# Kernel tuning notes

Hardware: AMD Instinct MI355X
Metric: run time of the kernel (lower is better)

The kernel has to match this reference:

```python
import jax, jax.numpy as jnp
import numpy as np

NBODY = 63          # body 0 = world, body 1 = free-joint root, bodies 2..62 = hinge
NHINGE = NBODY - 2  # 61 hinge dofs -> qpos dim = 7 + 61 = 68
NSITES = 16
B = 131072


def _qmul(q1, q2):
    """Hamilton product, (w,x,y,z) convention. Broadcasts over leading dims."""
    w1, x1, y1, z1 = q1[..., 0], q1[..., 1], q1[..., 2], q1[..., 3]
    w2, x2, y2, z2 = q2[..., 0], q2[..., 1], q2[..., 2], q2[..., 3]
    return jnp.stack([
        w1 * w2 - x1 * x2 - y1 * y2 - z1 * z2,
        w1 * x2 + x1 * w2 + y1 * z2 - z1 * y2,
        w1 * y2 - x1 * z2 + y1 * w2 + z1 * x2,
        w1 * z2 + x1 * y2 - y1 * x2 + z1 * w2,
    ], axis=-1)


def _qrot(q, v):
    """Rotate v by unit quaternion q (equivalent to q*v*q^-1 sandwich)."""
    u = q[..., 1:]
    w = q[..., :1]
    t = 2.0 * jnp.cross(u, v)
    return v + w * t + jnp.cross(u, t)


def setup_inputs() -> dict:
    key = jax.random.key(0)
    ks = jax.random.split(key, 8)
    qpos = jax.random.normal(ks[0], (B, 7 + NHINGE), dtype=jnp.float32) * 0.3
    body_pos = jax.random.normal(ks[1], (NBODY, 3), dtype=jnp.float32) * 0.1
    bq = jax.random.normal(ks[2], (NBODY, 4), dtype=jnp.float32)
    body_quat = bq / jnp.linalg.norm(bq, axis=-1, keepdims=True)
    ax = jax.random.normal(ks[3], (NHINGE, 3), dtype=jnp.float32)
    hinge_axis = ax / jnp.linalg.norm(ax, axis=-1, keepdims=True)
    jnt_pos = jax.random.normal(ks[4], (NHINGE, 3), dtype=jnp.float32) * 0.05
    site_pos = jax.random.normal(ks[5], (NSITES, 3), dtype=jnp.float32) * 0.05
    body_parent = jnp.maximum(jnp.arange(NBODY, dtype=jnp.int32) - 1, 0)  # chain tree
    site_body = jax.random.randint(ks[6], (NSITES,), 1, NBODY, dtype=jnp.int32)
    return {
        'qpos': qpos, 'body_pos': body_pos, 'body_quat': body_quat,
        'hinge_axis': hinge_axis, 'jnt_pos': jnt_pos, 'site_pos': site_pos,
        'body_parent': body_parent, 'site_body': site_body,
    }


def reference(qpos, body_pos, body_quat, hinge_axis, jnt_pos, site_pos,
              body_parent, site_body):
    # Structural ints are static tree topology: pull to host for Python indexing.
    parents = np.asarray(body_parent)
    sbody = np.asarray(site_body)
    Bn = qpos.shape[0]
    nbody = body_pos.shape[0]

    wp = [None] * nbody  # per-body world position [B,3]
    wq = [None] * nbody  # per-body world quaternion [B,4]
    wp[0] = jnp.zeros((Bn, 3), dtype=qpos.dtype)
    wq[0] = jnp.broadcast_to(jnp.array([1.0, 0.0, 0.0, 0.0], dtype=qpos.dtype), (Bn, 4))

    # body 1: free joint -> root pos + normalized quat straight from qpos
    wp[1] = qpos[:, 0:3]
    q = qpos[:, 3:7]
    wq[1] = q / jnp.linalg.norm(q, axis=-1, keepdims=True)

    # hinge bodies, parents always processed before children
    for bid in range(2, nbody):
        h = bid - 2
        p = int(parents[bid])
        half = 0.5 * qpos[:, 7 + h]
        s, c = jnp.sin(half), jnp.cos(half)
        ax = hinge_axis[h]
        hq = jnp.stack([c, s * ax[0], s * ax[1], s * ax[2]], axis=-1)  # [B,4]
        local_combined = _qmul(jnp.broadcast_to(body_quat[bid], (Bn, 4)), hq)
        anchor = wp[p] + _qrot(wq[p], body_pos[bid] + jnt_pos[h])  # world joint anchor
        nq = _qmul(wq[p], local_combined)
        wq[bid] = nq
        wp[bid] = anchor - _qrot(nq, jnt_pos[h])

    WP = jnp.stack(wp, axis=1)  # [B, nbody, 3]
    WQ = jnp.stack(wq, axis=1)  # [B, nbody, 4]

    # sites: vectorized gather + rotate over all keypoint sites at once
    sq = WQ[:, sbody]                         # [B, S, 4]
    sp = WP[:, sbody]                         # [B, S, 3]
    sites = sp + _qrot(sq, site_pos[None, :, :])  # [B, S, 3]
    return sites
```

## Files before the change

kernel.cpp:

```cpp
#include <hip/hip_runtime.h>


#define NBODY  63
#define NHINGE 61
#define NSITES 16
#define QDIM   68
#define LSTRIDE 49
#define INV2PI 0.15915494309189535f

typedef unsigned int u32;

#define HC_OFF   0
#define SP_OFF   (NHINGE * 16)
#define MASK_OFF (SP_OFF + NSITES * 4)
#define BM_OFF   (MASK_OFF + 64)

__global__ void fk_setup(const float* __restrict__ body_pos, const float* __restrict__ body_quat,
                         const float* __restrict__ hinge_axis, const float* __restrict__ jnt_pos,
                         const float* __restrict__ site_pos, const int* __restrict__ site_body,
                         float* __restrict__ ws)
{
    int tid = threadIdx.x;
    if (tid < NHINGE) {
        int h = tid, bid = h + 2;
        float uw = body_quat[bid*4+0], ux = body_quat[bid*4+1];
        float uy = body_quat[bid*4+2], uz = body_quat[bid*4+3];
        float ax = hinge_axis[h*3+0], ay = hinge_axis[h*3+1], az = hinge_axis[h*3+2];
        float jx = jnt_pos[h*3+0],   jy = jnt_pos[h*3+1],   jz = jnt_pos[h*3+2];
        float bx = body_pos[bid*3+0], by = body_pos[bid*3+1], bz = body_pos[bid*3+2];
        float* o = ws + HC_OFF + h * 16;
        o[0] = uw; o[1] = ux; o[2] = uy; o[3] = uz;
        o[4] = -(ux * ax + uy * ay + uz * az);
        o[5] =  uw * ax + uy * az - uz * ay;
        o[6] =  uw * ay - ux * az + uz * ax;
        o[7] =  uw * az + ux * ay - uy * ax;
        o[8] = bx + jx; o[9] = by + jy; o[10] = bz + jz; o[11] = 0.f;
        o[12] = jx; o[13] = jy; o[14] = jz; o[15] = 0.f;
    }
    if (tid < NSITES) {
        float* o = ws + SP_OFF + tid * 4;
        o[0] = site_pos[tid*3+0];
        o[1] = site_pos[tid*3+1];
        o[2] = site_pos[tid*3+2];
        o[3] = 0.f;
    }
    if (tid == 0) {
        int* im = (int*)(ws + MASK_OFF);
        unsigned long long bm = 0ull;
        for (int b = 0; b < NBODY; b++) {
            int m = 0;
            for (int s = 0; s < NSITES; s++)
                if (site_body[s] == b) m |= (1 << s);
            im[b] = m;
            if (m) bm |= (1ull << b);
        }
        u32* pbm = (u32*)(ws + BM_OFF);
        pbm[0] = (u32)bm; pbm[1] = (u32)(bm >> 32);
    }
}

__global__ __launch_bounds__(256, 3)
void fk_main(const float* __restrict__ qpos, const float* __restrict__ ws,
             float* __restrict__ out)
{
    __shared__ float sbuf[256 * LSTRIDE];
    const int tid = threadIdx.x;
    const int t = blockIdx.x * 256 + tid;
    float* my = sbuf + tid * LSTRIDE;
    const float* rowp = qpos + (size_t)t * QDIM;

    const u32* pbm = (const u32*)(ws + BM_OFF);
    unsigned long long bodymask = ((unsigned long long)pbm[1] << 32) | (unsigned long long)pbm[0];
    const int* im = (const int*)(ws + MASK_OFF);

    float4 r0 = *reinterpret_cast<const float4*>(rowp);
    float2 r1 = *reinterpret_cast<const float2*>(rowp + 4);
    float  r2 = rowp[6];
    float wpx = r0.x, wpy = r0.y, wpz = r0.z;
    float qw = r0.w, qx = r1.x, qy = r1.y, qz = r2;
    float inv = rsqrtf(qw * qw + qx * qx + qy * qy + qz * qz);
    qw *= inv; qx *= inv; qy *= inv; qz *= inv;

    auto emit = [&](int bid) {
        int m = im[bid];
        while (m) {
            int s = __ffs(m) - 1; m &= m - 1;
            const float* sp = ws + SP_OFF + s * 4;
            float vx = sp[0], vy = sp[1], vz = sp[2];
            float tx = 2.f * (qy * vz - qz * vy);
            float ty = 2.f * (qz * vx - qx * vz);
            float tz = 2.f * (qx * vy - qy * vx);
            float* o = my + s * 3;
            o[0] = wpx + vx + qw * tx + (qy * tz - qz * ty);
            o[1] = wpy + vy + qw * ty + (qz * tx - qx * tz);
            o[2] = wpz + vz + qw * tz + (qx * ty - qy * tx);
        }
    };

    if (bodymask & 2ull) emit(1);

    float ang = rowp[7];
#pragma unroll 1
    for (int h = 0; h < NHINGE; h++) {
        int nidx = 7 + ((h + 1 < NHINGE) ? (h + 1) : h);
        float angn = rowp[nidx];

        const float* c = ws + HC_OFF + h * 16;
        float rev = (0.5f * INV2PI) * ang;
        float sn = __builtin_amdgcn_sinf(rev);
        float cs = __builtin_amdgcn_cosf(rev);
        float lw = cs * c[0] + sn * c[4];
        float lx = cs * c[1] + sn * c[5];
        float ly = cs * c[2] + sn * c[6];
        float lz = cs * c[3] + sn * c[7];
        float ax = c[8], ay = c[9], az = c[10];
        float tx = 2.f * (qy * az - qz * ay);
        float ty = 2.f * (qz * ax - qx * az);
        float tz = 2.f * (qx * ay - qy * ax);
        float anx = wpx + ax + qw * tx + (qy * tz - qz * ty);
        float any_ = wpy + ay + qw * ty + (qz * tx - qx * tz);
        float anz = wpz + az + qw * tz + (qx * ty - qy * tx);
        float nw = qw * lw - qx * lx - qy * ly - qz * lz;
        float nx = qw * lx + qx * lw + qy * lz - qz * ly;
        float ny = qw * ly - qx * lz + qy * lw + qz * lx;
        float nz = qw * lz + qx * ly - qy * lx + qz * lw;
        float jx = c[12], jy = c[13], jz = c[14];
        float t2x = 2.f * (ny * jz - nz * jy);
        float t2y = 2.f * (nz * jx - nx * jz);
        float t2z = 2.f * (nx * jy - ny * jx);
        wpx = anx - (jx + nw * t2x + (ny * t2z - nz * t2y));
        wpy = any_ - (jy + nw * t2y + (nz * t2x - nx * t2z));
        wpz = anz - (jz + nw * t2z + (nx * t2y - ny * t2x));
        qw = nw; qx = nx; qy = ny; qz = nz;

        if ((bodymask >> (h + 2)) & 1ull) emit(h + 2);
        ang = angn;
    }

    __syncthreads();

    {
        size_t blk_dw = (size_t)blockIdx.x * (256 * 48);
        float4* out4 = reinterpret_cast<float4*>(out + blk_dw);
#pragma unroll
        for (int k = 0; k < 12; k++) {
            int g = k * 256 + tid;
            int q = g / 12;
            int r = (g - q * 12) * 4;
            const float* p = sbuf + q * LSTRIDE + r;
            float4 v = { p[0], p[1], p[2], p[3] };
            out4[g] = v;
        }
    }
}

extern "C" void kernel_launch(void* const* d_in, const int* in_sizes, int n_in,
                              void* d_out, int out_size, void* d_ws, size_t ws_size,
                              hipStream_t stream)
{
    const float* qpos       = (const float*)d_in[0];
    const float* body_pos   = (const float*)d_in[1];
    const float* body_quat  = (const float*)d_in[2];
    const float* hinge_axis = (const float*)d_in[3];
    const float* jnt_pos    = (const float*)d_in[4];
    const float* site_pos   = (const float*)d_in[5];
    const int* site_body    = (const int*)d_in[7];
    float* ws = (float*)d_ws;

    int nb = in_sizes[0] / QDIM;

    fk_setup<<<1, 64, 0, stream>>>(body_pos, body_quat, hinge_axis, jnt_pos,
                                   site_pos, site_body, ws);
    fk_main<<<nb / 256, 256, 0, stream>>>(qpos, ws, (float*)d_out);
}
```

Measured before the change: 145.1 us.

## Process two batch rows per thread with paired math and LDS-staged constants

Each thread now runs two independent kinematic chains (rows t and t+B/2), using a two-lane float pair type so the compiler can issue packed FP32 ops and overlap two dependency chains. Per-hinge constants are copied into shared memory once per block and software-prefetched two hinges ahead, and the hinge loop is unrolled by two. The block size drops to 128 threads with a single-block occupancy hint. Register pressure rises and there are half as many threads, so latency hiding now depends on instruction-level parallelism rather than occupancy.

```diff
diff --git a/kernel.cpp b/kernel.cpp
--- a/kernel.cpp
+++ b/kernel.cpp
@@ -5,6 +5,7 @@
 #define NHINGE 61
 #define NSITES 16
 #define QDIM   68
+#define NT     128
 #define LSTRIDE 49
 #define INV2PI 0.15915494309189535f
 
@@ -14,6 +15,14 @@
 #define SP_OFF   (NHINGE * 16)
 #define MASK_OFF (SP_OFF + NSITES * 4)
 #define BM_OFF   (MASK_OFF + 64)
+
+struct P { float a, b; };
+__device__ __forceinline__ P mk(float x, float y) { P r; r.a = x; r.b = y; return r; }
+__device__ __forceinline__ P bc(float x) { return mk(x, x); }
+__device__ __forceinline__ P operator+(P u, P v) { return mk(u.a + v.a, u.b + v.b); }
+__device__ __forceinline__ P operator-(P u, P v) { return mk(u.a - v.a, u.b - v.b); }
+__device__ __forceinline__ P operator*(P u, P v) { return mk(u.a * v.a, u.b * v.b); }
+__device__ __forceinline__ P operator*(P u, float s) { return mk(u.a * s, u.b * s); }
 
 __global__ void fk_setup(const float* __restrict__ body_pos, const float* __restrict__ body_quat,
                          const float* __restrict__ hinge_axis, const float* __restrict__ jnt_pos,
@@ -59,27 +68,39 @@
     }
 }
 
-__global__ __launch_bounds__(256, 3)
+__global__ __launch_bounds__(NT, 1)
 void fk_main(const float* __restrict__ qpos, const float* __restrict__ ws,
-             float* __restrict__ out)
+             float* __restrict__ out, int nb)
 {
-    __shared__ float sbuf[256 * LSTRIDE];
+    __shared__ float sbuf[2 * NT * LSTRIDE];
+    __shared__ float cbuf[NHINGE * 16];
     const int tid = threadIdx.x;
-    const int t = blockIdx.x * 256 + tid;
-    float* my = sbuf + tid * LSTRIDE;
-    const float* rowp = qpos + (size_t)t * QDIM;
+    const int tA = blockIdx.x * NT + tid;
+    const int tB = tA + (nb >> 1);
+    float* myA = sbuf + tid * LSTRIDE;
+    float* myB = sbuf + (NT + tid) * LSTRIDE;
+
+    for (int k = tid; k < NHINGE * 16; k += NT) cbuf[k] = ws[HC_OFF + k];
+    __syncthreads();
+
+    const float* rowA = qpos + (size_t)tA * QDIM;
+    const float* rowB = qpos + (size_t)tB * QDIM;
 
     const u32* pbm = (const u32*)(ws + BM_OFF);
     unsigned long long bodymask = ((unsigned long long)pbm[1] << 32) | (unsigned long long)pbm[0];
     const int* im = (const int*)(ws + MASK_OFF);
 
-    float4 r0 = *reinterpret_cast<const float4*>(rowp);
-    float2 r1 = *reinterpret_cast<const float2*>(rowp + 4);
-    float  r2 = rowp[6];
-    float wpx = r0.x, wpy = r0.y, wpz = r0.z;
-    float qw = r0.w, qx = r1.x, qy = r1.y, qz = r2;
-    float inv = rsqrtf(qw * qw + qx * qx + qy * qy + qz * qz);
-    qw *= inv; qx *= inv; qy *= inv; qz *= inv;
+    float4 ra = *reinterpret_cast<const float4*>(rowA);
+    float2 rb = *reinterpret_cast<const float2*>(rowA + 4);
+    float  rc = rowA[6];
+    float4 sa = *reinterpret_cast<const float4*>(rowB);
+    float2 sb = *reinterpret_cast<const float2*>(rowB + 4);
+    float  sc = rowB[6];
+    P wpx = mk(ra.x, sa.x), wpy = mk(ra.y, sa.y), wpz = mk(ra.z, sa.z);
+    P qw = mk(ra.w, sa.w), qx = mk(rb.x, sb.x), qy = mk(rb.y, sb.y), qz = mk(rc, sc);
+    P n2 = qw*qw + qx*qx + qy*qy + qz*qz;
+    P inv = mk(rsqrtf(n2.a), rsqrtf(n2.b));
+    qw = qw*inv; qx = qx*inv; qy = qy*inv; qz = qz*inv;
 
     auto emit = [&](int bid) {
         int m = im[bid];
@@ -87,69 +108,100 @@
             int s = __ffs(m) - 1; m &= m - 1;
             const float* sp = ws + SP_OFF + s * 4;
             float vx = sp[0], vy = sp[1], vz = sp[2];
-            float tx = 2.f * (qy * vz - qz * vy);
-            float ty = 2.f * (qz * vx - qx * vz);
-            float tz = 2.f * (qx * vy - qy * vx);
-            float* o = my + s * 3;
-            o[0] = wpx + vx + qw * tx + (qy * tz - qz * ty);
-            o[1] = wpy + vy + qw * ty + (qz * tx - qx * tz);
-            o[2] = wpz + vz + qw * tz + (qx * ty - qy * tx);
+            P tx = (qy*bc(vz) - qz*bc(vy)) * 2.f;
+            P ty = (qz*bc(vx) - qx*bc(vz)) * 2.f;
+            P tz = (qx*bc(vy) - qy*bc(vx)) * 2.f;
+            P ox = wpx + bc(vx) + qw*tx + (qy*tz - qz*ty);
+            P oy = wpy + bc(vy) + qw*ty + (qz*tx - qx*tz);
+            P oz = wpz + bc(vz) + qw*tz + (qx*ty - qy*tx);
+            float* oA = myA + s * 3;
+            float* oB = myB + s * 3;
+            oA[0] = ox.a; oA[1] = oy.a; oA[2] = oz.a;
+            oB[0] = ox.b; oB[1] = oy.b; oB[2] = oz.b;
         }
     };
 
     if (bodymask & 2ull) emit(1);
 
-    float ang = rowp[7];
+    auto step = [&](int h, const float4& c0, const float4& c1,
+                    const float4& c2, const float4& c3, P ang) {
+        P rev = ang * (0.5f * INV2PI);
+        P sn = mk(__builtin_amdgcn_sinf(rev.a), __builtin_amdgcn_sinf(rev.b));
+        P cs = mk(__builtin_amdgcn_cosf(rev.a), __builtin_amdgcn_cosf(rev.b));
+        P lw = cs*bc(c0.x) + sn*bc(c1.x);
+        P lx = cs*bc(c0.y) + sn*bc(c1.y);
+        P ly = cs*bc(c0.z) + sn*bc(c1.z);
+        P lz = cs*bc(c0.w) + sn*bc(c1.w);
+        float ax = c2.x, ay = c2.y, az = c2.z;
+        P tx = (qy*bc(az) - qz*bc(ay)) * 2.f;
+        P ty = (qz*bc(ax) - qx*bc(az)) * 2.f;
+        P tz = (qx*bc(ay) - qy*bc(ax)) * 2.f;
+        P anx = wpx + bc(ax) + qw*tx + (qy*tz - qz*ty);
+        P any_= wpy + bc(ay) + qw*ty + (qz*tx - qx*tz);
+        P anz = wpz + bc(az) + qw*tz + (qx*ty - qy*tx);
+        P nw = qw*lw - qx*lx - qy*ly - qz*lz;
+        P nx = qw*lx + qx*lw + qy*lz - qz*ly;
+        P ny = qw*ly - qx*lz + qy*lw + qz*lx;
+        P nz = qw*lz + qx*ly - qy*lx + qz*lw;
+        float jx = c3.x, jy = c3.y, jz = c3.z;
+        P t2x = (ny*bc(jz) - nz*bc(jy)) * 2.f;
+        P t2y = (nz*bc(jx) - nx*bc(jz)) * 2.f;
+        P t2z = (nx*bc(jy) - ny*bc(jx)) * 2.f;
+        wpx = anx - (bc(jx) + nw*t2x + (ny*t2z - nz*t2y));
+        wpy = any_ - (bc(jy) + nw*t2y + (nz*t2x - nx*t2z));
+        wpz = anz - (bc(jz) + nw*t2z + (nx*t2y - ny*t2x));
+        qw = nw; qx = nx; qy = ny; qz = nz;
+        if ((bodymask >> (h + 2)) & 1ull) emit(h + 2);
+    };
+
+    auto ldc = [&](int h, float4& d0, float4& d1, float4& d2, float4& d3) {
+        const float4* p = reinterpret_cast<const float4*>(cbuf + h * 16);
+        d0 = p[0]; d1 = p[1]; d2 = p[2]; d3 = p[3];
+    };
+
+    float4 ea0, ea1, ea2, ea3, eb0, eb1, eb2, eb3;
+    ldc(0, ea0, ea1, ea2, ea3);
+    ldc(1, eb0, eb1, eb2, eb3);
+    P angE = mk(rowA[7], rowB[7]);
+    P angO = mk(rowA[8], rowB[8]);
+
 #pragma unroll 1
-    for (int h = 0; h < NHINGE; h++) {
-        int nidx = 7 + ((h + 1 < NHINGE) ? (h + 1) : h);
-        float angn = rowp[nidx];
-
-        const float* c = ws + HC_OFF + h * 16;
-        float rev = (0.5f * INV2PI) * ang;
-        float sn = __builtin_amdgcn_sinf(rev);
-        float cs = __builtin_amdgcn_cosf(rev);
-        float lw = cs * c[0] + sn * c[4];
-        float lx = cs * c[1] + sn * c[5];
-        float ly = cs * c[2] + sn * c[6];
-        float lz = cs * c[3] + sn * c[7];
-        float ax = c[8], ay = c[9], az = c[10];
-        float tx = 2.f * (qy * az - qz * ay);
-        float ty = 2.f * (qz * ax - qx * az);
-        float tz = 2.f * (qx * ay - qy * ax);
-        float anx = wpx + ax + qw * tx + (qy * tz - qz * ty);
-        float any_ = wpy + ay + qw * ty + (qz * tx - qx * tz);
-        float anz = wpz + az + qw * tz + (qx * ty - qy * tx);
-        float nw = qw * lw - qx * lx - qy * ly - qz * lz;
-        float nx = qw * lx + qx * lw + qy * lz - qz * ly;
-        float ny = qw * ly - qx * lz + qy * lw + qz * lx;
-        float nz = qw * lz + qx * ly - qy * lx + qz * lw;
-        float jx = c[12], jy = c[13], jz = c[14];
-        float t2x = 2.f * (ny * jz - nz * jy);
-        float t2y = 2.f * (nz * jx - nx * jz);
-        float t2z = 2.f * (nx * jy - ny * jx);
-        wpx = anx - (jx + nw * t2x + (ny * t2z - nz * t2y));
-        wpy = any_ - (jy + nw * t2y + (nz * t2x - nx * t2z));
-        wpz = anz - (jz + nw * t2z + (nx * t2y - ny * t2x));
-        qw = nw; qx = nx; qy = ny; qz = nz;
-
-        if ((bodymask >> (h + 2)) & 1ull) emit(h + 2);
-        ang = angn;
-    }
+    for (int h = 0; h < 60; h += 2) {
+        int h2 = h + 2;
+        int h3 = (h + 3 < NHINGE) ? (h + 3) : (NHINGE - 1);
+        float4 na0, na1, na2, na3, nb0, nb1, nb2, nb3;
+        ldc(h2, na0, na1, na2, na3);
+        ldc(h3, nb0, nb1, nb2, nb3);
+        P nAngE = mk(rowA[7 + h2], rowB[7 + h2]);
+        P nAngO = mk(rowA[7 + h3], rowB[7 + h3]);
+
+        step(h,     ea0, ea1, ea2, ea3, angE);
+        step(h + 1, eb0, eb1, eb2, eb3, angO);
+
+        ea0 = na0; ea1 = na1; ea2 = na2; ea3 = na3;
+        eb0 = nb0; eb1 = nb1; eb2 = nb2; eb3 = nb3;
+        angE = nAngE; angO = nAngO;
+    }
+    step(60, ea0, ea1, ea2, ea3, angE);
 
     __syncthreads();
 
     {
-        size_t blk_dw = (size_t)blockIdx.x * (256 * 48);
-        float4* out4 = reinterpret_cast<float4*>(out + blk_dw);
+        size_t baseA = (size_t)(blockIdx.x * NT) * 48;
+        size_t baseB = baseA + (size_t)(nb >> 1) * 48;
+        float4* outA = reinterpret_cast<float4*>(out + baseA);
+        float4* outB = reinterpret_cast<float4*>(out + baseB);
 #pragma unroll
         for (int k = 0; k < 12; k++) {
-            int g = k * 256 + tid;
+            int g = k * NT + tid;
             int q = g / 12;
             int r = (g - q * 12) * 4;
-            const float* p = sbuf + q * LSTRIDE + r;
-            float4 v = { p[0], p[1], p[2], p[3] };
-            out4[g] = v;
+            const float* pA = sbuf + q * LSTRIDE + r;
+            const float* pB = sbuf + (NT + q) * LSTRIDE + r;
+            float4 vA = { pA[0], pA[1], pA[2], pA[3] };
+            float4 vB = { pB[0], pB[1], pB[2], pB[3] };
+            outA[g] = vA;
+            outB[g] = vB;
         }
     }
 }
@@ -171,5 +223,5 @@
 
     fk_setup<<<1, 64, 0, stream>>>(body_pos, body_quat, hinge_axis, jnt_pos,
                                    site_pos, site_body, ws);
-    fk_main<<<nb / 256, 256, 0, stream>>>(qpos, ws, (float*)d_out);
+    fk_main<<<(nb / 2) / NT, NT, 0, stream>>>(qpos, ws, (float*)d_out, nb);
 }
```

Measured after the change: 146.0 us. Within noise of the previous version (+0.6%).

## Split hinge chain across four lanes with parallel prefix composition of transforms

Applied to the files above, without the earlier changes.

Each batch element is now handled by four lanes, and each lane composes a segment of about 16 hinge transforms as rigid transforms relative to identity. The segments are combined with a shuffle-based prefix scan, and each lane's recorded site positions are then fixed up by its prefix transform. Hinge constants move into shared memory and the block now covers 64 elements. The intent is to shorten the serial dependency chain and raise parallelism. In exchange it adds extra composition work, site fixups, and lane imbalance from the 16/16/16/13 segment split.

```diff
diff --git a/kernel.cpp b/kernel.cpp
--- a/kernel.cpp
+++ b/kernel.cpp
@@ -5,7 +5,9 @@
 #define NHINGE 61
 #define NSITES 16
 #define QDIM   68
-#define LSTRIDE 49
+#define NT     256
+#define EPB    64
+#define EST    52
 #define INV2PI 0.15915494309189535f
 
 typedef unsigned int u32;
@@ -14,6 +16,23 @@
 #define SP_OFF   (NHINGE * 16)
 #define MASK_OFF (SP_OFF + NSITES * 4)
 #define BM_OFF   (MASK_OFF + 64)
+
+struct X { float qw, qx, qy, qz, tx, ty, tz; };
+
+__device__ __forceinline__ X xcompose(const X& A, const X& B) {
+    X r;
+    r.qw = A.qw*B.qw - A.qx*B.qx - A.qy*B.qy - A.qz*B.qz;
+    r.qx = A.qw*B.qx + A.qx*B.qw + A.qy*B.qz - A.qz*B.qy;
+    r.qy = A.qw*B.qy - A.qx*B.qz + A.qy*B.qw + A.qz*B.qx;
+    r.qz = A.qw*B.qz + A.qx*B.qy - A.qy*B.qx + A.qz*B.qw;
+    float cx = 2.f*(A.qy*B.tz - A.qz*B.ty);
+    float cy = 2.f*(A.qz*B.tx - A.qx*B.tz);
+    float cz = 2.f*(A.qx*B.ty - A.qy*B.tx);
+    r.tx = B.tx + A.qw*cx + (A.qy*cz - A.qz*cy) + A.tx;
+    r.ty = B.ty + A.qw*cy + (A.qz*cx - A.qx*cz) + A.ty;
+    r.tz = B.tz + A.qw*cz + (A.qx*cy - A.qy*cx) + A.tz;
+    return r;
+}
 
 __global__ void fk_setup(const float* __restrict__ body_pos, const float* __restrict__ body_quat,
                          const float* __restrict__ hinge_axis, const float* __restrict__ jnt_pos,
@@ -59,95 +78,142 @@
     }
 }
 
-__global__ __launch_bounds__(256, 3)
+__global__ __launch_bounds__(NT, 4)
 void fk_main(const float* __restrict__ qpos, const float* __restrict__ ws,
              float* __restrict__ out)
 {
-    __shared__ float sbuf[256 * LSTRIDE];
-    const int tid = threadIdx.x;
-    const int t = blockIdx.x * 256 + tid;
-    float* my = sbuf + tid * LSTRIDE;
-    const float* rowp = qpos + (size_t)t * QDIM;
-
-    const u32* pbm = (const u32*)(ws + BM_OFF);
-    unsigned long long bodymask = ((unsigned long long)pbm[1] << 32) | (unsigned long long)pbm[0];
-    const int* im = (const int*)(ws + MASK_OFF);
-
-    float4 r0 = *reinterpret_cast<const float4*>(rowp);
-    float2 r1 = *reinterpret_cast<const float2*>(rowp + 4);
-    float  r2 = rowp[6];
-    float wpx = r0.x, wpy = r0.y, wpz = r0.z;
-    float qw = r0.w, qx = r1.x, qy = r1.y, qz = r2;
-    float inv = rsqrtf(qw * qw + qx * qx + qy * qy + qz * qz);
-    qw *= inv; qx *= inv; qy *= inv; qz *= inv;
-
-    auto emit = [&](int bid) {
-        int m = im[bid];
+    __shared__ float cbuf[NHINGE * 16];
+    __shared__ float spbuf[NSITES * 4];
+    __shared__ int   smask[64];
+    __shared__ float stag[EPB * EST];
+
+    const int tid  = threadIdx.x;
+    const int lane = tid & 63;
+    const int k    = tid & 3;
+    const int eloc = tid >> 2;
+    const int start = k * 16;
+    const int len   = (k < 3) ? 16 : 13;
+
+    for (int i = tid; i < NHINGE * 16; i += NT) cbuf[i] = ws[HC_OFF + i];
+    if (tid < NSITES * 4) spbuf[tid] = ws[SP_OFF + tid];
+    if (tid < 63) smask[tid] = ((const int*)(ws + MASK_OFF))[tid];
+    __syncthreads();
+
+    const float* rowp = qpos + (size_t)(blockIdx.x * EPB + eloc) * QDIM;
+    float* my = stag + eloc * EST;
+
+    float f[16];
+#pragma unroll
+    for (int i = 0; i < 16; i++) { f[i] = 0.f; if (i < len) f[i] = rowp[7 + start + i]; }
+
+    X s = {1.f, 0.f, 0.f, 0.f, 0.f, 0.f, 0.f};
+    int mysites = 0;
+
+    auto record = [&](int m) {
+        mysites |= m;
         while (m) {
-            int s = __ffs(m) - 1; m &= m - 1;
-            const float* sp = ws + SP_OFF + s * 4;
-            float vx = sp[0], vy = sp[1], vz = sp[2];
-            float tx = 2.f * (qy * vz - qz * vy);
-            float ty = 2.f * (qz * vx - qx * vz);
-            float tz = 2.f * (qx * vy - qy * vx);
-            float* o = my + s * 3;
-            o[0] = wpx + vx + qw * tx + (qy * tz - qz * ty);
-            o[1] = wpy + vy + qw * ty + (qz * tx - qx * tz);
-            o[2] = wpz + vz + qw * tz + (qx * ty - qy * tx);
+            int si = __ffs(m) - 1; m &= m - 1;
+            float vx = spbuf[si*4+0], vy = spbuf[si*4+1], vz = spbuf[si*4+2];
+            float cx = 2.f*(s.qy*vz - s.qz*vy);
+            float cy = 2.f*(s.qz*vx - s.qx*vz);
+            float cz = 2.f*(s.qx*vy - s.qy*vx);
+            float* o = my + si * 3;
+            o[0] = vx + s.qw*cx + (s.qy*cz - s.qz*cy) + s.tx;
+            o[1] = vy + s.qw*cy + (s.qz*cx - s.qx*cz) + s.ty;
+            o[2] = vz + s.qw*cz + (s.qx*cy - s.qy*cx) + s.tz;
         }
     };
 
-    if (bodymask & 2ull) emit(1);
-
-    float ang = rowp[7];
-#pragma unroll 1
-    for (int h = 0; h < NHINGE; h++) {
-        int nidx = 7 + ((h + 1 < NHINGE) ? (h + 1) : h);
-        float angn = rowp[nidx];
-
-        const float* c = ws + HC_OFF + h * 16;
-        float rev = (0.5f * INV2PI) * ang;
-        float sn = __builtin_amdgcn_sinf(rev);
-        float cs = __builtin_amdgcn_cosf(rev);
-        float lw = cs * c[0] + sn * c[4];
-        float lx = cs * c[1] + sn * c[5];
-        float ly = cs * c[2] + sn * c[6];
-        float lz = cs * c[3] + sn * c[7];
-        float ax = c[8], ay = c[9], az = c[10];
-        float tx = 2.f * (qy * az - qz * ay);
-        float ty = 2.f * (qz * ax - qx * az);
-        float tz = 2.f * (qx * ay - qy * ax);
-        float anx = wpx + ax + qw * tx + (qy * tz - qz * ty);
-        float any_ = wpy + ay + qw * ty + (qz * tx - qx * tz);
-        float anz = wpz + az + qw * tz + (qx * ty - qy * tx);
-        float nw = qw * lw - qx * lx - qy * ly - qz * lz;
-        float nx = qw * lx + qx * lw + qy * lz - qz * ly;
-        float ny = qw * ly - qx * lz + qy * lw + qz * lx;
-        float nz = qw * lz + qx * ly - qy * lx + qz * lw;
-        float jx = c[12], jy = c[13], jz = c[14];
-        float t2x = 2.f * (ny * jz - nz * jy);
-        float t2y = 2.f * (nz * jx - nx * jz);
-        float t2z = 2.f * (nx * jy - ny * jx);
-        wpx = anx - (jx + nw * t2x + (ny * t2z - nz * t2y));
-        wpy = any_ - (jy + nw * t2y + (nz * t2x - nx * t2z));
-        wpz = anz - (jz + nw * t2z + (nx * t2y - ny * t2x));
-        qw = nw; qx = nx; qy = ny; qz = nz;
-
-        if ((bodymask >> (h + 2)) & 1ull) emit(h + 2);
-        ang = angn;
+    if (k == 0) {
+        float4 r0 = *reinterpret_cast<const float4*>(rowp);
+        float2 r1 = *reinterpret_cast<const float2*>(rowp + 4);
+        float  r2 = rowp[6];
+        float inv = rsqrtf(r0.w*r0.w + r1.x*r1.x + r1.y*r1.y + r2*r2);
+        s.qw = r0.w*inv; s.qx = r1.x*inv; s.qy = r1.y*inv; s.qz = r2*inv;
+        s.tx = r0.x; s.ty = r0.y; s.tz = r0.z;
+        int m1 = smask[1];
+        if (m1) record(m1);
+    }
+
+#pragma unroll
+    for (int i = 0; i < 16; i++) {
+        if (i < len) {
+            int h = start + i;
+            const float4* cp = reinterpret_cast<const float4*>(cbuf + h * 16);
+            float4 c0 = cp[0], c1 = cp[1], c2 = cp[2], c3 = cp[3];
+            float rev = f[i] * (0.5f * INV2PI);
+            float sn = __builtin_amdgcn_sinf(rev);
+            float cs = __builtin_amdgcn_cosf(rev);
+            float lw = cs*c0.x + sn*c1.x;
+            float lx = cs*c0.y + sn*c1.y;
+            float ly = cs*c0.z + sn*c1.z;
+            float lz = cs*c0.w + sn*c1.w;
+            float jx = c3.x, jy = c3.y, jz = c3.z;
+            float cx = 2.f*(ly*jz - lz*jy);
+            float cy = 2.f*(lz*jx - lx*jz);
+            float cz = 2.f*(lx*jy - ly*jx);
+            float thx = c2.x - (jx + lw*cx + (ly*cz - lz*cy));
+            float thy = c2.y - (jy + lw*cy + (lz*cx - lx*cz));
+            float thz = c2.z - (jz + lw*cz + (lx*cy - ly*cx));
+            float dx = 2.f*(s.qy*thz - s.qz*thy);
+            float dy = 2.f*(s.qz*thx - s.qx*thz);
+            float dz = 2.f*(s.qx*thy - s.qy*thx);
+            s.tx += thx + s.qw*dx + (s.qy*dz - s.qz*dy);
+            s.ty += thy + s.qw*dy + (s.qz*dx - s.qx*dz);
+            s.tz += thz + s.qw*dz + (s.qx*dy - s.qy*dx);
+            float nw = s.qw*lw - s.qx*lx - s.qy*ly - s.qz*lz;
+            float nx = s.qw*lx + s.qx*lw + s.qy*lz - s.qz*ly;
+            float ny = s.qw*ly - s.qx*lz + s.qy*lw + s.qz*lx;
+            float nz = s.qw*lz + s.qx*ly - s.qy*lx + s.qz*lw;
+            s.qw = nw; s.qx = nx; s.qy = ny; s.qz = nz;
+            int m = smask[h + 2];
+            if (m) record(m);
+        }
+    }
+
+    X x = s;
+#pragma unroll
+    for (int d = 1; d <= 2; d <<= 1) {
+        int src = lane - d; if (src < 0) src = lane;
+        X y;
+        y.qw = __shfl(x.qw, src); y.qx = __shfl(x.qx, src);
+        y.qy = __shfl(x.qy, src); y.qz = __shfl(x.qz, src);
+        y.tx = __shfl(x.tx, src); y.ty = __shfl(x.ty, src); y.tz = __shfl(x.tz, src);
+        if (k >= d) x = xcompose(y, x);
+    }
+    X P;
+    {
+        int src = lane - 1; if (src < 0) src = lane;
+        P.qw = __shfl(x.qw, src); P.qx = __shfl(x.qx, src);
+        P.qy = __shfl(x.qy, src); P.qz = __shfl(x.qz, src);
+        P.tx = __shfl(x.tx, src); P.ty = __shfl(x.ty, src); P.tz = __shfl(x.tz, src);
+    }
+
+    if (k > 0) {
+        int m = mysites;
+        while (m) {
+            int si = __ffs(m) - 1; m &= m - 1;
+            float* o = my + si * 3;
+            float vx = o[0], vy = o[1], vz = o[2];
+            float cx = 2.f*(P.qy*vz - P.qz*vy);
+            float cy = 2.f*(P.qz*vx - P.qx*vz);
+            float cz = 2.f*(P.qx*vy - P.qy*vx);
+            o[0] = vx + P.qw*cx + (P.qy*cz - P.qz*cy) + P.tx;
+            o[1] = vy + P.qw*cy + (P.qz*cx - P.qx*cz) + P.ty;
+            o[2] = vz + P.qw*cz + (P.qx*cy - P.qy*cx) + P.tz;
+        }
     }
 
     __syncthreads();
 
     {
-        size_t blk_dw = (size_t)blockIdx.x * (256 * 48);
-        float4* out4 = reinterpret_cast<float4*>(out + blk_dw);
-#pragma unroll
-        for (int k = 0; k < 12; k++) {
-            int g = k * 256 + tid;
+        float4* out4 = reinterpret_cast<float4*>(out + (size_t)blockIdx.x * (EPB * 48));
+#pragma unroll
+        for (int j = 0; j < 3; j++) {
+            int g = j * NT + tid;
             int q = g / 12;
             int r = (g - q * 12) * 4;
-            const float* p = sbuf + q * LSTRIDE + r;
+            const float* p = stag + q * EST + r;
             float4 v = { p[0], p[1], p[2], p[3] };
             out4[g] = v;
         }
@@ -171,5 +237,5 @@
 
     fk_setup<<<1, 64, 0, stream>>>(body_pos, body_quat, hinge_axis, jnt_pos,
                                    site_pos, site_body, ws);
-    fk_main<<<nb / 256, 256, 0, stream>>>(qpos, ws, (float*)d_out);
-}
+    fk_main<<<nb / EPB, NT, 0, stream>>>(qpos, ws, (float*)d_out);
+}
```

After: 137.4 us. -5.3%, faster.
